# Kernel tuning notes

Hardware: AMD Instinct MI355X
Metric: run time of the kernel (lower is better)

## Reference

```python
import jax, jax.numpy as jnp
import numpy as np

N = 50000   # nodes
E = 800000  # edges (avg degree 16)
D = 2048    # resnet50 feature dim
C = 256     # layer_size
NEG_SLOPE = 0.2


def setup_inputs() -> dict:
    key = jax.random.key(0)
    ks = jax.random.split(key, 16)
    s = 0.02
    inp = {
        'x': jax.random.normal(ks[0], (N, D), jnp.float32),
        'edge_index': jax.random.randint(ks[1], (2, E), 0, N, dtype=jnp.int32),
        # GATConv layer 1 (in=D, out=C, heads=1)
        'W1': jax.random.normal(ks[2], (D, C), jnp.float32) * s,
        'a_src1': jax.random.normal(ks[3], (C,), jnp.float32) * s,
        'a_dst1': jax.random.normal(ks[4], (C,), jnp.float32) * s,
        'b1': jnp.zeros((C,), jnp.float32),
        # GATConv layer 2 (in=C, out=C)
        'W2': jax.random.normal(ks[5], (C, C), jnp.float32) * s,
        'a_src2': jax.random.normal(ks[6], (C,), jnp.float32) * s,
        'a_dst2': jax.random.normal(ks[7], (C,), jnp.float32) * s,
        'b2': jnp.zeros((C,), jnp.float32),
        # EdgePredictor: lin1 (2C -> C), lin2 (C -> 1)
        'Wp1': jax.random.normal(ks[8], (2 * C, C), jnp.float32) * s,
        'bp1': jnp.zeros((C,), jnp.float32),
        'wp2': jax.random.normal(ks[9], (C,), jnp.float32) * s,
        'bp2': jnp.zeros((), jnp.float32),
    }
    return inp


def gat_layer(x, src, dst, W, a_src, a_dst, b, n_nodes):
    # PyG GATConv, heads=1, concat=True: message flows src -> dst,
    # softmax over incoming edges of each dst node.
    h = x @ W                                   # [N, C]
    e = jax.nn.leaky_relu((h @ a_src)[src] + (h @ a_dst)[dst], NEG_SLOPE)  # [E]
    emax = jax.ops.segment_max(e, dst, num_segments=n_nodes)
    ex = jnp.exp(e - emax[dst])
    denom = jax.ops.segment_sum(ex, dst, num_segments=n_nodes)
    alpha = ex / (denom[dst] + 1e-16)           # [E]
    out = jax.ops.segment_sum(h[src] * alpha[:, None], dst, num_segments=n_nodes)
    return out + b


def reference(x, edge_index, W1, a_src1, a_dst1, b1, W2, a_src2, a_dst2, b2,
              Wp1, bp1, wp2, bp2):
    src, dst = edge_index[0], edge_index[1]
    # GATConv default add_self_loops=True
    loops = jnp.arange(N, dtype=src.dtype)
    src_sl = jnp.concatenate([src, loops])
    dst_sl = jnp.concatenate([dst, loops])

    h = gat_layer(x, src_sl, dst_sl, W1, a_src1, a_dst1, b1, N)
    h = gat_layer(h, src_sl, dst_sl, W2, a_src2, a_dst2, b2, N)

    # edge predictor on the ORIGINAL edge_index (no self loops)
    xe = jnp.concatenate([h[src], h[dst]], axis=-1)       # [E, 2C]
    z = jax.nn.relu(xe @ Wp1 + bp1)                        # [E, C]  (dropout: eval mode)
    return z @ wp2 + bp2                                   # [E]
```

## Files before the change

### kernel.cpp

```cpp
#include <hip/hip_runtime.h>
#include <hip/hip_bf16.h>
#include <stdint.h>

#define NNODES 50000
#define NEDGES 800000
#define DIN    2048
#define CDIM   256
#define ELOOP  (NEDGES + NNODES)
#define DCAP   96

using bf16x8 = __attribute__((ext_vector_type(8))) short;
using f32x4  = __attribute__((ext_vector_type(4))) float;
using gvoid  = __attribute__((address_space(1))) const void;
using lvoid  = __attribute__((address_space(3))) void;

__device__ __forceinline__ float bf2f(uint16_t u) {
    union { uint32_t i; float f; } v; v.i = (uint32_t)u << 16; return v.f;
}
__device__ __forceinline__ uint16_t f2bf(float f) {
    union { float f; uint32_t i; } v; v.f = f;
    uint32_t i = v.i;
    return (uint16_t)((i + 0x7FFFu + ((i >> 16) & 1u)) >> 16);
}
__device__ __forceinline__ void unpack8(uint4 r, float* f) {
    f[0] = bf2f((uint16_t)(r.x & 0xffffu)); f[1] = bf2f((uint16_t)(r.x >> 16));
    f[2] = bf2f((uint16_t)(r.y & 0xffffu)); f[3] = bf2f((uint16_t)(r.y >> 16));
    f[4] = bf2f((uint16_t)(r.z & 0xffffu)); f[5] = bf2f((uint16_t)(r.z >> 16));
    f[6] = bf2f((uint16_t)(r.w & 0xffffu)); f[7] = bf2f((uint16_t)(r.w >> 16));
}

#define BM 128
#define BN 128
#define BK 32

#define WAITVM(N) asm volatile("s_waitcnt vmcnt(" #N ")" ::: "memory")

#define ROWDOT_EPILOGUE()                                                     \
    if (s_src) {                                                              \
        float av[4], dv[4];                                                   \
        for (int nt2 = 0; nt2 < 4; ++nt2) {                                   \
            int gn = bn + wn + nt2 * 16 + lm;                                 \
            av[nt2] = asrc[gn];                                               \
            dv[nt2] = adst[gn];                                               \
        }                                                                     \
        for (int mt = 0; mt < 4; ++mt)                                        \
            for (int r = 0; r < 4; ++r) {                                     \
                float ps = 0.f, pd = 0.f;                                     \
                for (int nt2 = 0; nt2 < 4; ++nt2) {                           \
                    float v = acc[mt][nt2][r];                                \
                    ps += v * av[nt2];                                        \
                    pd += v * dv[nt2];                                        \
                }                                                             \
                for (int d = 1; d < 16; d <<= 1) {                            \
                    ps += __shfl_xor(ps, d);                                  \
                    pd += __shfl_xor(pd, d);                                  \
                }                                                             \
                if (lm == 0) {                                                \
                    int gm = bm + wm + mt * 16 + lq * 4 + r;                  \
                    if (gm < M) {                                             \
                        atomicAdd(&s_src[gm], ps);                            \
                        atomicAdd(&s_dst[gm], pd);                            \
                    }                                                         \
                }                                                             \
            }                                                                 \
    }

__global__ __launch_bounds__(256)
void gemm_bt(const uint16_t* __restrict__ A, const uint16_t* __restrict__ Bt,
             uint16_t* __restrict__ C, const float* __restrict__ bias,
             const float* __restrict__ asrc, const float* __restrict__ adst,
             float* __restrict__ s_src, float* __restrict__ s_dst,
             int M, int N, int K)
{
    __shared__ __align__(16) uint16_t lA[3][BM * BK];
    __shared__ __align__(16) uint16_t lB[3][BN * BK];
    const int tid  = threadIdx.x;
    const int wave = tid >> 6;
    const int lane = tid & 63;
    const int lm = lane & 15, lq = lane >> 4;
    const int bm = blockIdx.x * BM;
    const int bn = blockIdx.y * BN;
    const int wm = (wave >> 1) * 64;
    const int wn = (wave & 1) * 64;

    f32x4 acc[4][4];
    for (int i = 0; i < 4; ++i)
        for (int j = 0; j < 4; ++j)
            acc[i][j] = (f32x4)0.0f;

    auto stage = [&](int buf, int k0) {
        for (int j = 0; j < 2; ++j) {
            int c = j * 256 + wave * 64 + lane;
            int row = c >> 2, cc = c & 3;
            int gr = bm + row; if (gr >= M) gr = M - 1;
            const uint16_t* gp = A + (size_t)gr * K + k0 + cc * 8;
            __builtin_amdgcn_global_load_lds((gvoid*)gp,
                (lvoid*)(lA[buf] + (size_t)(j * 256 + wave * 64) * 8), 16, 0, 0);
        }
        for (int j = 0; j < 2; ++j) {
            int c = j * 256 + wave * 64 + lane;
            int row = c >> 2, cc = c & 3;
            const uint16_t* gp = Bt + (size_t)(bn + row) * K + k0 + cc * 8;
            __builtin_amdgcn_global_load_lds((gvoid*)gp,
                (lvoid*)(lB[buf] + (size_t)(j * 256 + wave * 64) * 8), 16, 0, 0);
        }
    };

    const int ntiles = K / BK;
    stage(0, 0);
    stage(1, BK);
    WAITVM(4);
    __builtin_amdgcn_s_barrier();

    for (int t = 0; t < ntiles; ++t) {
        const int cur = t % 3;
        if (t + 2 < ntiles) stage((t + 2) % 3, (t + 2) * BK);

        bf16x8 af[4], bfr[4];
        for (int mt = 0; mt < 4; ++mt)
            af[mt] = *(const bf16x8*)(lA[cur] + (wm + mt * 16 + lm) * BK + lq * 8);
        for (int nt2 = 0; nt2 < 4; ++nt2)
            bfr[nt2] = *(const bf16x8*)(lB[cur] + (wn + nt2 * 16 + lm) * BK + lq * 8);

        for (int mt = 0; mt < 4; ++mt)
            for (int nt2 = 0; nt2 < 4; ++nt2)
                acc[mt][nt2] = __builtin_amdgcn_mfma_f32_16x16x32_bf16(
                    af[mt], bfr[nt2], acc[mt][nt2], 0, 0, 0);

        if (t + 1 < ntiles) {
            if (t + 2 < ntiles) WAITVM(4);
            else                WAITVM(0);
            __builtin_amdgcn_s_barrier();
        }
    }

    for (int mt = 0; mt < 4; ++mt) {
        for (int nt2 = 0; nt2 < 4; ++nt2) {
            int gn = bn + wn + nt2 * 16 + lm;
            float badd = bias ? bias[gn] : 0.0f;
            for (int r = 0; r < 4; ++r) {
                int gm = bm + wm + mt * 16 + lq * 4 + r;
                if (gm < M)
                    C[(size_t)gm * N + gn] = f2bf(acc[mt][nt2][r] + badd);
            }
        }
    }

    ROWDOT_EPILOGUE();
}

__global__ __launch_bounds__(256)
void gemm_f32_bt(const float* __restrict__ A, const uint16_t* __restrict__ Bt,
                 uint16_t* __restrict__ C,
                 const float* __restrict__ asrc, const float* __restrict__ adst,
                 float* __restrict__ s_src, float* __restrict__ s_dst,
                 int M, int N, int K)
{
    __shared__ __align__(16) float    lA[3][BM * BK];
    __shared__ __align__(16) uint16_t lB[3][BN * BK];
    const int tid  = threadIdx.x;
    const int wave = tid >> 6;
    const int lane = tid & 63;
    const int lm = lane & 15, lq = lane >> 4;
    const int bm = blockIdx.x * BM;
    const int bn = blockIdx.y * BN;
    const int wm = (wave >> 1) * 64;
    const int wn = (wave & 1) * 64;

    f32x4 acc[4][4];
    for (int i = 0; i < 4; ++i)
        for (int j = 0; j < 4; ++j)
            acc[i][j] = (f32x4)0.0f;

    auto stage = [&](int buf, int k0) {
        for (int j = 0; j < 4; ++j) {
            int c = j * 256 + wave * 64 + lane;
            int row = c >> 3;
            int lc  = (c & 7) ^ (row & 7);
            int gr = bm + row; if (gr >= M) gr = M - 1;
            const float* gp = A + (size_t)gr * K + k0 + lc * 4;
            __builtin_amdgcn_global_load_lds((gvoid*)gp,
                (lvoid*)(lA[buf] + (size_t)(j * 256 + wave * 64) * 4), 16, 0, 0);
        }
        for (int j = 0; j < 2; ++j) {
            int c = j * 256 + wave * 64 + lane;
            int row = c >> 2, cc = c & 3;
            const uint16_t* gp = Bt + (size_t)(bn + row) * K + k0 + cc * 8;
            __builtin_amdgcn_global_load_lds((gvoid*)gp,
                (lvoid*)(lB[buf] + (size_t)(j * 256 + wave * 64) * 8), 16, 0, 0);
        }
    };

    const int ntiles = K / BK;
    stage(0, 0);
    stage(1, BK);
    WAITVM(6);
    __builtin_amdgcn_s_barrier();

    for (int t = 0; t < ntiles; ++t) {
        const int cur = t % 3;
        if (t + 2 < ntiles) stage((t + 2) % 3, (t + 2) * BK);

        bf16x8 af[4], bfr[4];
        for (int mt = 0; mt < 4; ++mt) {
            int r = wm + mt * 16 + lm;
            int s0 = (lq * 2)     ^ (r & 7);
            int s1 = (lq * 2 + 1) ^ (r & 7);
            f32x4 a0 = *(const f32x4*)(lA[cur] + r * BK + s0 * 4);
            f32x4 a1 = *(const f32x4*)(lA[cur] + r * BK + s1 * 4);
            union { uint32_t u[4]; bf16x8 v; } t2;
            float x0 = a0[0], x1 = a0[1], x2 = a0[2], x3 = a0[3];
            float y0 = a1[0], y1 = a1[1], y2 = a1[2], y3 = a1[3];
            asm("v_cvt_pk_bf16_f32 %0, %1, %2" : "=v"(t2.u[0]) : "v"(x0), "v"(x1));
            asm("v_cvt_pk_bf16_f32 %0, %1, %2" : "=v"(t2.u[1]) : "v"(x2), "v"(x3));
            asm("v_cvt_pk_bf16_f32 %0, %1, %2" : "=v"(t2.u[2]) : "v"(y0), "v"(y1));
            asm("v_cvt_pk_bf16_f32 %0, %1, %2" : "=v"(t2.u[3]) : "v"(y2), "v"(y3));
            af[mt] = t2.v;
        }
        for (int nt2 = 0; nt2 < 4; ++nt2)
            bfr[nt2] = *(const bf16x8*)(lB[cur] + (wn + nt2 * 16 + lm) * BK + lq * 8);

        for (int mt = 0; mt < 4; ++mt)
            for (int nt2 = 0; nt2 < 4; ++nt2)
                acc[mt][nt2] = __builtin_amdgcn_mfma_f32_16x16x32_bf16(
                    af[mt], bfr[nt2], acc[mt][nt2], 0, 0, 0);

        if (t + 1 < ntiles) {
            if (t + 2 < ntiles) WAITVM(6);
            else                WAITVM(0);
            __builtin_amdgcn_s_barrier();
        }
    }

    for (int mt = 0; mt < 4; ++mt) {
        for (int nt2 = 0; nt2 < 4; ++nt2) {
            int gn = bn + wn + nt2 * 16 + lm;
            for (int r = 0; r < 4; ++r) {
                int gm = bm + wm + mt * 16 + lq * 4 + r;
                if (gm < M)
                    C[(size_t)gm * N + gn] = f2bf(acc[mt][nt2][r]);
            }
        }
    }

    ROWDOT_EPILOGUE();
}

__global__ __launch_bounds__(256)
void transpose_cvt4_kernel(const float* __restrict__ W1,
                           const float* __restrict__ W2,
                           const float* __restrict__ Wp1,
                           uint16_t* __restrict__ W1t,
                           uint16_t* __restrict__ W2t,
                           uint16_t* __restrict__ WpABt)
{
    __shared__ float tile[32][33];
    const int z = blockIdx.z;
    const float* W; uint16_t* Wt; int K, N;
    if (z == 0)      { W = W1;                Wt = W1t;                K = DIN;  N = CDIM; }
    else if (z == 1) { W = W2;                Wt = W2t;                K = CDIM; N = CDIM; }
    else if (z == 2) { W = Wp1;               Wt = WpABt;              K = CDIM; N = CDIM; }
    else             { W = Wp1 + CDIM * CDIM; Wt = WpABt + CDIM * CDIM; K = CDIM; N = CDIM; }
    const int k0 = blockIdx.x * 32, n0 = blockIdx.y * 32;
    if (k0 >= K) return;
    const int tx = threadIdx.x & 31, ty = threadIdx.x >> 5;
    for (int r = 0; r < 32; r += 8)
        tile[ty + r][tx] = W[(size_t)(k0 + ty + r) * N + n0 + tx];
    __syncthreads();
    for (int r = 0; r < 32; r += 8)
        Wt[(size_t)(n0 + ty + r) * K + k0 + tx] = f2bf(tile[tx][ty + r]);
}

__global__ void bias512_kernel(const float* __restrict__ bp1,
                               float* __restrict__ bias512)
{
    int i = blockIdx.x * 256 + threadIdx.x;
    if (i < 512) bias512[i] = (i < 256) ? bp1[i] : 0.0f;
}

__global__ void count_kernel(const int* __restrict__ ei, int* __restrict__ rs)
{
    int i = blockIdx.x * 256 + threadIdx.x;
    if (i >= ELOOP) return;
    int dst = (i < NEDGES) ? ei[NEDGES + i] : (i - NEDGES);
    atomicAdd(&rs[dst + 1], 1);
}

__global__ __launch_bounds__(1024)
void scan_part_kernel(int* __restrict__ rs, int* __restrict__ bsum)
{
    __shared__ int wsum[16];
    const int b = blockIdx.x, tid = threadIdx.x, lane = tid & 63, w = tid >> 6;
    int i = b * 1024 + tid;
    int v = (i <= NNODES) ? rs[i] : 0;
    int s = v;
    for (int d = 1; d < 64; d <<= 1) {
        int t = __shfl_up(s, d);
        if (lane >= d) s += t;
    }
    if (lane == 63) wsum[w] = s;
    __syncthreads();
    if (tid < 16) {
        int x = wsum[tid];
        for (int d = 1; d < 16; d <<= 1) {
            int t = __shfl_up(x, d);
            if (tid >= d) x += t;
        }
        wsum[tid] = x;
    }
    __syncthreads();
    int incl = s + (w > 0 ? wsum[w - 1] : 0);
    if (i <= NNODES) rs[i] = incl;
    if (tid == 1023) bsum[b] = incl;
}

__global__ void scan_bsum_kernel(int* __restrict__ bsum, int nb)
{
    int tid = threadIdx.x;
    int v = (tid < nb) ? bsum[tid] : 0;
    for (int d = 1; d < 64; d <<= 1) {
        int t = __shfl_up(v, d);
        if (tid >= d) v += t;
    }
    if (tid < nb) bsum[tid] = v;
}

__global__ __launch_bounds__(1024)
void scan_add_kernel(const int* __restrict__ bsum, int* __restrict__ rs,
                     int* __restrict__ cursor)
{
    int b = blockIdx.x;
    int i = b * 1024 + threadIdx.x;
    int add = b ? bsum[b - 1] : 0;
    if (i <= NNODES) {
        int r = rs[i] + add;
        rs[i] = r;
        if (i < NNODES) cursor[i] = r;
    }
}

__global__ void fill_kernel(const int* __restrict__ ei, int* __restrict__ cursor,
                            int* __restrict__ csr_src, int* __restrict__ csr_eid)
{
    int i = blockIdx.x * 256 + threadIdx.x;
    if (i >= ELOOP) return;
    int src, dst, eid;
    if (i < NEDGES) { src = ei[i]; dst = ei[NEDGES + i]; eid = i; }
    else            { src = dst = i - NEDGES; eid = -1; }
    int pos = atomicAdd(&cursor[dst], 1);
    csr_src[pos] = src;
    csr_eid[pos] = eid;
}

__global__ __launch_bounds__(256)
void attn_kernel(const int* __restrict__ row_start, const int* __restrict__ csr_src,
                 const float* __restrict__ s_src, const float* __restrict__ s_dst,
                 const uint16_t* __restrict__ g, const float* __restrict__ bvec,
                 uint16_t* __restrict__ hout)
{
    __shared__ int   lsrc[4][DCAP];
    __shared__ float le[4][DCAP];
    const int w = threadIdx.x >> 6;
    int n = blockIdx.x * 4 + w;
    int lane = threadIdx.x & 63;
    int beg = row_start[n], end = row_start[n + 1];
    int deg = end - beg;
    float sdn = s_dst[n];

    float m = -1e30f;
    for (int idx = lane; idx < deg; idx += 64) {
        int src = csr_src[beg + idx];
        float e = s_src[src] + sdn;
        e = (e > 0.f) ? e : 0.2f * e;
        if (idx < DCAP) { lsrc[w][idx] = src; le[w][idx] = e; }
        m = fmaxf(m, e);
    }
    for (int d = 32; d; d >>= 1) m = fmaxf(m, __shfl_xor(m, d));
    asm volatile("s_waitcnt lgkmcnt(0)" ::: "memory");

    float sum = 0.f;
    for (int idx = lane; idx < deg; idx += 64) {
        float e;
        if (idx < DCAP) e = le[w][idx];
        else {
            int src = csr_src[beg + idx];
            e = s_src[src] + sdn;
            e = (e > 0.f) ? e : 0.2f * e;
        }
        sum += __expf(e - m);
    }
    for (int d = 32; d; d >>= 1) sum += __shfl_xor(sum, d);
    float inv = 1.f / (sum + 1e-16f);

    const int gq = lane >> 3, gl = lane & 7;
    float a[32];
    #pragma unroll
    for (int j = 0; j < 32; ++j) a[j] = 0.f;

    for (int idx = gq; idx < deg; idx += 8) {
        int src; float e;
        if (idx < DCAP) { src = lsrc[w][idx]; e = le[w][idx]; }
        else {
            src = csr_src[beg + idx];
            e = s_src[src] + sdn;
            e = (e > 0.f) ? e : 0.2f * e;
        }
        float alpha = __expf(e - m) * inv;
        const uint16_t* gp = g + (size_t)src * CDIM + gl * 32;
        uint4 r0 = *(const uint4*)gp;
        uint4 r1 = *(const uint4*)(gp + 8);
        uint4 r2 = *(const uint4*)(gp + 16);
        uint4 r3 = *(const uint4*)(gp + 24);
        float f0[8], f1[8], f2[8], f3[8];
        unpack8(r0, f0); unpack8(r1, f1); unpack8(r2, f2); unpack8(r3, f3);
        #pragma unroll
        for (int j = 0; j < 8; ++j) {
            a[j]      += alpha * f0[j];
            a[8 + j]  += alpha * f1[j];
            a[16 + j] += alpha * f2[j];
            a[24 + j] += alpha * f3[j];
        }
    }
    #pragma unroll
    for (int j = 0; j < 32; ++j) {
        a[j] += __shfl_xor(a[j], 8);
        a[j] += __shfl_xor(a[j], 16);
        a[j] += __shfl_xor(a[j], 32);
    }

    if (gq == 0) {
        uint16_t* op = hout + (size_t)n * CDIM + gl * 32;
        #pragma unroll
        for (int blk = 0; blk < 4; ++blk) {
            const float4 ba = *(const float4*)(bvec + gl * 32 + blk * 8);
            const float4 bb = *(const float4*)(bvec + gl * 32 + blk * 8 + 4);
            uint4 o;
            o.x = (uint32_t)f2bf(a[blk*8+0] + ba.x) | ((uint32_t)f2bf(a[blk*8+1] + ba.y) << 16);
            o.y = (uint32_t)f2bf(a[blk*8+2] + ba.z) | ((uint32_t)f2bf(a[blk*8+3] + ba.w) << 16);
            o.z = (uint32_t)f2bf(a[blk*8+4] + bb.x) | ((uint32_t)f2bf(a[blk*8+5] + bb.y) << 16);
            o.w = (uint32_t)f2bf(a[blk*8+6] + bb.z) | ((uint32_t)f2bf(a[blk*8+7] + bb.w) << 16);
            *(uint4*)(op + blk * 8) = o;
        }
    }
}

__global__ __launch_bounds__(256)
void edgepred_kernel(const int* __restrict__ row_start,
                     const int* __restrict__ csr_src,
                     const int* __restrict__ csr_eid,
                     const uint16_t* __restrict__ UV,
                     const float* __restrict__ wp2, const float* __restrict__ bp2,
                     float* __restrict__ out)
{
    int n = blockIdx.x * 4 + (threadIdx.x >> 6);
    int lane = threadIdx.x & 63;
    int q = lane >> 4, ql = lane & 15;
    int beg = row_start[n], end = row_start[n + 1];

    const uint16_t* vp = UV + (size_t)n * 512 + 256 + ql * 16;
    uint4 v0 = *(const uint4*)vp;
    uint4 v1 = *(const uint4*)(vp + 8);
    float v[16];
    unpack8(v0, v); unpack8(v1, v + 8);
    float wv[16];
    #pragma unroll
    for (int j = 0; j < 16; j += 4) {
        float4 wq = *(const float4*)(wp2 + ql * 16 + j);
        wv[j] = wq.x; wv[j+1] = wq.y; wv[j+2] = wq.z; wv[j+3] = wq.w;
    }
    const float bp = *bp2;

    for (int i = beg + q; i < end; i += 4) {
        int eid = csr_eid[i];
        if (eid < 0) continue;
        int src = csr_src[i];
        const uint16_t* up = UV + (size_t)src * 512 + ql * 16;
        uint4 u0 = *(const uint4*)up;
        uint4 u1 = *(const uint4*)(up + 8);
        float u[16];
        unpack8(u0, u); unpack8(u1, u + 8);
        float acc = 0.f;
        #pragma unroll
        for (int j = 0; j < 16; ++j)
            acc += fmaxf(u[j] + v[j], 0.f) * wv[j];
        for (int d = 1; d < 16; d <<= 1) acc += __shfl_xor(acc, d);
        if (ql == 0) out[eid] = acc + bp;
    }
}

extern "C" void kernel_launch(void* const* d_in, const int* in_sizes, int n_in,
                              void* d_out, int out_size, void* d_ws, size_t ws_size,
                              hipStream_t stream)
{
    const float* x   = (const float*)d_in[0];
    const int*   ei  = (const int*)d_in[1];
    const float* W1  = (const float*)d_in[2];
    const float* as1 = (const float*)d_in[3];
    const float* ad1 = (const float*)d_in[4];
    const float* b1  = (const float*)d_in[5];
    const float* W2  = (const float*)d_in[6];
    const float* as2 = (const float*)d_in[7];
    const float* ad2 = (const float*)d_in[8];
    const float* b2  = (const float*)d_in[9];
    const float* Wp1 = (const float*)d_in[10];
    const float* bp1 = (const float*)d_in[11];
    const float* wp2 = (const float*)d_in[12];
    const float* bp2 = (const float*)d_in[13];
    float* out = (float*)d_out;

    char* ws = (char*)d_ws;
    size_t off = 0;
    auto alloc = [&](size_t bytes) -> void* {
        void* p = ws + off;
        off += (bytes + 255) & ~(size_t)255;
        return p;
    };
    uint16_t* W1t   = (uint16_t*)alloc((size_t)DIN * CDIM * 2);
    uint16_t* W2t   = (uint16_t*)alloc((size_t)CDIM * CDIM * 2);
    uint16_t* WpABt = (uint16_t*)alloc((size_t)2 * CDIM * CDIM * 2);
    int* row_start = (int*)alloc((NNODES + 1) * sizeof(int));
    int* cursor    = (int*)alloc(NNODES * sizeof(int));
    int* csr_src   = (int*)alloc((size_t)ELOOP * sizeof(int));
    int* csr_eid   = (int*)alloc((size_t)ELOOP * sizeof(int));
    int* bsum      = (int*)alloc(64 * sizeof(int));
    float* sbuf    = (float*)alloc((size_t)2 * NNODES * sizeof(float));
    float* s_src   = sbuf;
    float* s_dst   = sbuf + NNODES;
    float* bias512 = (float*)alloc(512 * sizeof(float));
    uint16_t* H    = (uint16_t*)alloc((size_t)NNODES * CDIM * 2);
    uint16_t* G    = (uint16_t*)alloc((size_t)NNODES * CDIM * 2);
    uint16_t* Vb   = (uint16_t*)alloc((size_t)NNODES * CDIM * 2);
    (void)Vb;
    uint16_t* UV   = G;

    hipMemsetAsync(row_start, 0, (NNODES + 1) * sizeof(int), stream);
    hipMemsetAsync(sbuf, 0, (size_t)2 * NNODES * sizeof(float), stream);

    transpose_cvt4_kernel<<<dim3(DIN / 32, CDIM / 32, 4), 256, 0, stream>>>(
        W1, W2, Wp1, W1t, W2t, WpABt);
    bias512_kernel<<<2, 256, 0, stream>>>(bp1, bias512);

    const int NB = (NNODES + 1 + 1023) / 1024;
    count_kernel<<<(ELOOP + 255) / 256, 256, 0, stream>>>(ei, row_start);
    scan_part_kernel<<<NB, 1024, 0, stream>>>(row_start, bsum);
    scan_bsum_kernel<<<1, 64, 0, stream>>>(bsum, NB);
    scan_add_kernel<<<NB, 1024, 0, stream>>>(bsum, row_start, cursor);
    fill_kernel<<<(ELOOP + 255) / 256, 256, 0, stream>>>(ei, cursor, csr_src, csr_eid);

    dim3 gg((NNODES + BM - 1) / BM, CDIM / BN);

    gemm_f32_bt<<<gg, 256, 0, stream>>>(x, W1t, G, as1, ad1, s_src, s_dst,
                                        NNODES, CDIM, DIN);
    attn_kernel<<<NNODES / 4, 256, 0, stream>>>(row_start, csr_src, s_src, s_dst, G, b1, H);

    hipMemsetAsync(sbuf, 0, (size_t)2 * NNODES * sizeof(float), stream);
    gemm_bt<<<gg, 256, 0, stream>>>(H, W2t, G, nullptr, as2, ad2, s_src, s_dst,
                                    NNODES, CDIM, CDIM);
    attn_kernel<<<NNODES / 4, 256, 0, stream>>>(row_start, csr_src, s_src, s_dst, G, b2, H);

    dim3 gg2((NNODES + BM - 1) / BM, 512 / BN);
    gemm_bt<<<gg2, 256, 0, stream>>>(H, WpABt, UV, bias512, nullptr, nullptr,
                                     nullptr, nullptr, NNODES, 512, CDIM);

    edgepred_kernel<<<NNODES / 4, 256, 0, stream>>>(row_start, csr_src, csr_eid,
                                                    UV, wp2, bp2, out);
}
```

Baseline: 1.082 ms.

## Split-K the first-layer GEMM with fp32 atomics and a separate rowdot finalize

Result: slower. 1.105 ms (+2.1%).

```diff
diff --git a/kernel.cpp b/kernel.cpp
--- a/kernel.cpp
+++ b/kernel.cpp
@@ -8,6 +8,7 @@
 #define CDIM   256
 #define ELOOP  (NEDGES + NNODES)
 #define DCAP   96
+#define SPLITK 4
 
 using bf16x8 = __attribute__((ext_vector_type(8))) short;
 using f32x4  = __attribute__((ext_vector_type(4))) float;
@@ -150,11 +151,8 @@
 }
 
 __global__ __launch_bounds__(256)
-void gemm_f32_bt(const float* __restrict__ A, const uint16_t* __restrict__ Bt,
-                 uint16_t* __restrict__ C,
-                 const float* __restrict__ asrc, const float* __restrict__ adst,
-                 float* __restrict__ s_src, float* __restrict__ s_dst,
-                 int M, int N, int K)
+void gemm_f32_bt_sk(const float* __restrict__ A, const uint16_t* __restrict__ Bt,
+                    float* __restrict__ C32, int M, int N, int K)
 {
     __shared__ __align__(16) float    lA[3][BM * BK];
     __shared__ __align__(16) uint16_t lB[3][BN * BK];
@@ -164,6 +162,7 @@
     const int lm = lane & 15, lq = lane >> 4;
     const int bm = blockIdx.x * BM;
     const int bn = blockIdx.y * BN;
+    const int kb = blockIdx.z * (K / SPLITK);
     const int wm = (wave >> 1) * 64;
     const int wn = (wave & 1) * 64;
 
@@ -191,15 +190,15 @@
         }
     };
 
-    const int ntiles = K / BK;
-    stage(0, 0);
-    stage(1, BK);
+    const int ntiles = (K / SPLITK) / BK;
+    stage(0, kb);
+    stage(1, kb + BK);
     WAITVM(6);
     __builtin_amdgcn_s_barrier();
 
     for (int t = 0; t < ntiles; ++t) {
         const int cur = t % 3;
-        if (t + 2 < ntiles) stage((t + 2) % 3, (t + 2) * BK);
+        if (t + 2 < ntiles) stage((t + 2) % 3, kb + (t + 2) * BK);
 
         bf16x8 af[4], bfr[4];
         for (int mt = 0; mt < 4; ++mt) {
@@ -238,12 +237,31 @@
             for (int r = 0; r < 4; ++r) {
                 int gm = bm + wm + mt * 16 + lq * 4 + r;
                 if (gm < M)
-                    C[(size_t)gm * N + gn] = f2bf(acc[mt][nt2][r]);
+                    atomicAdd(&C32[(size_t)gm * N + gn], acc[mt][nt2][r]);
             }
         }
     }
-
-    ROWDOT_EPILOGUE();
+}
+
+__global__ __launch_bounds__(256)
+void finalize_rowdot_kernel(const float* __restrict__ C32,
+                            const float* __restrict__ asrc,
+                            const float* __restrict__ adst,
+                            uint16_t* __restrict__ G,
+                            float* __restrict__ s_src, float* __restrict__ s_dst)
+{
+    int n = blockIdx.x * 4 + (threadIdx.x >> 6);
+    int lane = threadIdx.x & 63;
+    float4 c = *(const float4*)(C32 + (size_t)n * CDIM + lane * 4);
+    float4 av = *(const float4*)(asrc + lane * 4);
+    float4 dv = *(const float4*)(adst + lane * 4);
+    float a = c.x * av.x + c.y * av.y + c.z * av.z + c.w * av.w;
+    float b = c.x * dv.x + c.y * dv.y + c.z * dv.z + c.w * dv.w;
+    for (int d = 32; d; d >>= 1) { a += __shfl_xor(a, d); b += __shfl_xor(b, d); }
+    ushort4 o;
+    o.x = f2bf(c.x); o.y = f2bf(c.y); o.z = f2bf(c.z); o.w = f2bf(c.w);
+    *(ushort4*)(G + (size_t)n * CDIM + lane * 4) = o;
+    if (lane == 0) { s_src[n] = a; s_dst[n] = b; }
 }
 
 __global__ __launch_bounds__(256)
@@ -527,6 +545,7 @@
     float* s_src   = sbuf;
     float* s_dst   = sbuf + NNODES;
     float* bias512 = (float*)alloc(512 * sizeof(float));
+    float* C32     = (float*)alloc((size_t)NNODES * CDIM * sizeof(float));
     uint16_t* H    = (uint16_t*)alloc((size_t)NNODES * CDIM * 2);
     uint16_t* G    = (uint16_t*)alloc((size_t)NNODES * CDIM * 2);
     uint16_t* Vb   = (uint16_t*)alloc((size_t)NNODES * CDIM * 2);
@@ -534,7 +553,7 @@
     uint16_t* UV   = G;
 
     hipMemsetAsync(row_start, 0, (NNODES + 1) * sizeof(int), stream);
-    hipMemsetAsync(sbuf, 0, (size_t)2 * NNODES * sizeof(float), stream);
+    hipMemsetAsync(C32, 0, (size_t)NNODES * CDIM * sizeof(float), stream);
 
     transpose_cvt4_kernel<<<dim3(DIN / 32, CDIM / 32, 4), 256, 0, stream>>>(
         W1, W2, Wp1, W1t, W2t, WpABt);
@@ -549,8 +568,10 @@
 
     dim3 gg((NNODES + BM - 1) / BM, CDIM / BN);
 
-    gemm_f32_bt<<<gg, 256, 0, stream>>>(x, W1t, G, as1, ad1, s_src, s_dst,
-                                        NNODES, CDIM, DIN);
+    dim3 gsk((NNODES + BM - 1) / BM, CDIM / BN, SPLITK);
+    gemm_f32_bt_sk<<<gsk, 256, 0, stream>>>(x, W1t, C32, NNODES, CDIM, DIN);
+    finalize_rowdot_kernel<<<NNODES / 4, 256, 0, stream>>>(C32, as1, ad1, G,
+                                                           s_src, s_dst);
     attn_kernel<<<NNODES / 4, 256, 0, stream>>>(row_start, csr_src, s_src, s_dst, G, b1, H);
 
     hipMemsetAsync(sbuf, 0, (size_t)2 * NNODES * sizeof(float), stream);
```
